# Optimization experiments

Measured on AMD Instinct MI355X. Metric: run time of the kernel, lower is better.

Reference implementation:

```python
import jax, jax.numpy as jnp
import numpy as np

B, S, D, H, HD = 1, 4096, 768, 12, 64
L, C, WIN, NCLS = 2, 256, 256, 64
NC = S // C
V, FF = 50265, 3072
NEG = -1e9
SCALE = np.float32(1.0 / np.sqrt(HD))


def setup_inputs() -> dict:
    key = jax.random.key(0)
    ks = jax.random.split(key, 32)
    p = lambda k, shape: (0.02 * jax.random.normal(k, shape)).astype(jnp.float32)
    inp = {
        'x': jax.random.randint(ks[0], (B, S), 0, V, dtype=jnp.int32),
        'mask_src': jnp.ones((B, S), dtype=jnp.int32),
        'clss': jnp.sort(jax.random.randint(ks[1], (B, NCLS), 0, S, dtype=jnp.int32), axis=-1),
        'segs': jax.random.randint(ks[2], (B, S), 0, 2, dtype=jnp.int32),
        'word_emb': p(ks[3], (V, D)),
        'pos_emb': p(ks[4], (S, D)),
        'type_emb': p(ks[5], (2, D)),
        'ln_e_s': jnp.ones((D,), jnp.float32), 'ln_e_b': jnp.zeros((D,), jnp.float32),
        'Wq': p(ks[6], (L, D, D)), 'bq': jnp.zeros((L, D), jnp.float32),
        'Wk': p(ks[7], (L, D, D)), 'bk': jnp.zeros((L, D), jnp.float32),
        'Wv': p(ks[8], (L, D, D)), 'bv': jnp.zeros((L, D), jnp.float32),
        'Wqg': p(ks[9], (L, D, D)), 'bqg': jnp.zeros((L, D), jnp.float32),
        'Wkg': p(ks[10], (L, D, D)), 'bkg': jnp.zeros((L, D), jnp.float32),
        'Wvg': p(ks[11], (L, D, D)), 'bvg': jnp.zeros((L, D), jnp.float32),
        'Wo': p(ks[12], (L, D, D)), 'bo': jnp.zeros((L, D), jnp.float32),
        'ln1_s': jnp.ones((L, D), jnp.float32), 'ln1_b': jnp.zeros((L, D), jnp.float32),
        'Wf1': p(ks[13], (L, D, FF)), 'bf1': jnp.zeros((L, FF), jnp.float32),
        'Wf2': p(ks[14], (L, FF, D)), 'bf2': jnp.zeros((L, D), jnp.float32),
        'ln2_s': jnp.ones((L, D), jnp.float32), 'ln2_b': jnp.zeros((L, D), jnp.float32),
    }
    return inp


def _layer_norm(x, s, b):
    m = jnp.mean(x, -1, keepdims=True)
    v = jnp.mean((x - m) ** 2, -1, keepdims=True)
    return (x - m) * jax.lax.rsqrt(v + 1e-5) * s + b


def _forward(x, mask_src, clss, segs, word_emb, pos_emb, type_emb, ln_e_s, ln_e_b,
             Wq, bq, Wk, bk, Wv, bv, Wqg, bqg, Wkg, bkg, Wvg, bvg, Wo, bo,
             ln1_s, ln1_b, Wf1, bf1, Wf2, bf2, ln2_s, ln2_b):
    # global positions: union of all clss values, same for every batch row
    g_idx = clss.reshape(-1)                                       # [NCLS]
    is_glb = jnp.zeros((S,), bool).at[g_idx].set(True)             # [S]
    kvalid = (mask_src > 0) & (~is_glb)[None, :]                   # band keys: no pad, no global
    gi = (jnp.arange(NC) * C)[:, None] + jnp.arange(3 * C)[None, :]  # gather idx into padded seq
    rel = jnp.arange(3 * C)[None, :] - (jnp.arange(C)[:, None] + C)  # key offset from query
    band_ok = jnp.abs(rel) <= WIN                                   # [C,3C]
    kv3 = jnp.pad(kvalid, ((0, 0), (C, C)))[:, gi]                  # [B,NC,3C]
    bmask = band_ok[None, None, None, :, :] & kv3[:, None, :, None, :]  # [B,1,NC,C,3C]
    gkey_ok = (mask_src[:, g_idx] > 0)[:, None, None, :]            # [B,1,1,NCLS]
    full_ok = (mask_src > 0)[:, None, None, :]                      # [B,1,1,S]

    h = _layer_norm(word_emb[x] + pos_emb[jnp.arange(S)][None] + type_emb[segs], ln_e_s, ln_e_b)

    for l in range(L):
        q = ((h @ Wq[l] + bq[l]).reshape(B, S, H, HD)) * SCALE
        k = (h @ Wk[l] + bk[l]).reshape(B, S, H, HD)
        v = (h @ Wv[l] + bv[l]).reshape(B, S, H, HD)
        # --- sliding-window band attention ---
        k3 = jnp.pad(k, ((0, 0), (C, C), (0, 0), (0, 0)))[:, gi]    # [B,NC,3C,H,HD]
        v3 = jnp.pad(v, ((0, 0), (C, C), (0, 0), (0, 0)))[:, gi]
        qc = q.reshape(B, NC, C, H, HD)
        sb = jnp.einsum('bnqhd,bnkhd->bhnqk', qc, k3)               # [B,H,NC,C,3C]
        sb = jnp.where(bmask, sb, NEG)
        # --- global keys seen by every query ---
        kg, vg = k[:, g_idx], v[:, g_idx]                           # [B,NCLS,H,HD]
        sg = jnp.einsum('bshd,bkhd->bhsk', q, kg)                   # [B,H,S,NCLS]
        sg = jnp.where(gkey_ok, sg, NEG)
        scores = jnp.concatenate([sg, sb.reshape(B, H, S, 3 * C)], -1)
        probs = jax.nn.softmax(scores, axis=-1)
        pg = probs[..., :NCLS]
        pb = probs[..., NCLS:].reshape(B, H, NC, C, 3 * C)
        out = jnp.einsum('bhnqk,bnkhd->bnqhd', pb, v3).reshape(B, S, H, HD)
        out = out + jnp.einsum('bhsk,bkhd->bshd', pg, vg)
        # --- global query tokens: full attention with *_global projections ---
        hg = h[:, g_idx]                                            # [B,NCLS,D]
        qg = ((hg @ Wqg[l] + bqg[l]).reshape(B, NCLS, H, HD)) * SCALE
        kgf = (h @ Wkg[l] + bkg[l]).reshape(B, S, H, HD)
        vgf = (h @ Wvg[l] + bvg[l]).reshape(B, S, H, HD)
        sfull = jnp.einsum('bqhd,bkhd->bhqk', qg, kgf)              # [B,H,NCLS,S]
        sfull = jnp.where(full_ok, sfull, NEG)
        og = jnp.einsum('bhqk,bkhd->bqhd', jax.nn.softmax(sfull, -1), vgf)
        out = out.at[:, g_idx].set(og)
        # --- output proj, residual, LN, FFN ---
        attn_out = out.reshape(B, S, D) @ Wo[l] + bo[l]
        h = _layer_norm(h + attn_out, ln1_s[l], ln1_b[l])
        ff = jax.nn.gelu(h @ Wf1[l] + bf1[l]) @ Wf2[l] + bf2[l]
        h = _layer_norm(h + ff, ln2_s[l], ln2_b[l])
    return h


def reference(x, mask_src, clss, segs, word_emb, pos_emb, type_emb, ln_e_s, ln_e_b,
              Wq, bq, Wk, bk, Wv, bv, Wqg, bqg, Wkg, bkg, Wvg, bvg, Wo, bo,
              ln1_s, ln1_b, Wf1, bf1, Wf2, bf2, ln2_s, ln2_b):
    return _forward(x, mask_src, clss, segs, word_emb, pos_emb, type_emb, ln_e_s, ln_e_b,
                    Wq, bq, Wk, bk, Wv, bv, Wqg, bqg, Wkg, bkg, Wvg, bvg, Wo, bo,
                    ln1_s, ln1_b, Wf1, bf1, Wf2, bf2, ln2_s, ln2_b)
```

## Files before the change

kernel.cpp:

```cpp
#include <hip/hip_runtime.h>
#include <hip/hip_bf16.h>
#include <cstdint>

#define SEQ  4096
#define DIM  768
#define NH   12
#define HDIM 64
#define NLAYER 2
#define CHK  256
#define WINR 256
#define NCLS 64
#define NCHK 16
#define FFD  3072
#define QSCALE 0.125f
#define LOG2E 1.44269504f
#define QSC2 (QSCALE * LOG2E)
#define SD ((size_t)SEQ * DIM)
#define PS_LD 72
#define TK 64

typedef __attribute__((__vector_size__(16))) float floatx4;
typedef __attribute__((ext_vector_type(8))) __bf16 bf16x8;
typedef __attribute__((ext_vector_type(4))) __bf16 bf16x4;

__device__ __forceinline__ void async16(const void* g, void* l) {
    __builtin_amdgcn_global_load_lds(
        (const __attribute__((address_space(1))) uint32_t*)g,
        (__attribute__((address_space(3))) uint32_t*)l, 16, 0, 0);
}

__device__ __forceinline__ float gelu_f(float x) {
    float x3 = x * x * x;
    return 0.5f * x * (1.0f + tanhf(0.7978845608028654f * (x + 0.044715f * x3)));
}

__global__ __launch_bounds__(64) void set_rank_kernel(
    const int* __restrict__ clss, int* __restrict__ isglb)
{
    isglb[clss[threadIdx.x]] = 1;
}

__global__ __launch_bounds__(256) void embed_ln_kernel(
    const int* __restrict__ x, const int* __restrict__ segs,
    const float* __restrict__ word_emb, const float* __restrict__ pos_emb,
    const float* __restrict__ type_emb, const float* __restrict__ gs,
    const float* __restrict__ gb, float* __restrict__ h, __bf16* __restrict__ hb,
    int* __restrict__ isglb)
{
    int wave = threadIdx.x >> 6, lane = threadIdx.x & 63;
    int s = blockIdx.x * 4 + wave;
    if (lane == 0) isglb[s] = 0;
    int w = x[s], sg = segs[s];
    const float4* wp = (const float4*)(word_emb + (size_t)w * DIM);
    const float4* pp = (const float4*)(pos_emb + (size_t)s * DIM);
    const float4* tp = (const float4*)(type_emb + (size_t)sg * DIM);
    float4 v[3]; float lsum = 0.f;
    #pragma unroll
    for (int i = 0; i < 3; i++) {
        int d4 = lane + i * 64;
        float4 a = wp[d4], b = pp[d4], c = tp[d4];
        float4 r;
        r.x = a.x + b.x + c.x; r.y = a.y + b.y + c.y;
        r.z = a.z + b.z + c.z; r.w = a.w + b.w + c.w;
        v[i] = r; lsum += r.x + r.y + r.z + r.w;
    }
    #pragma unroll
    for (int st = 32; st > 0; st >>= 1) lsum += __shfl_xor(lsum, st);
    float mean = lsum * (1.0f / DIM);
    float lv = 0.f;
    #pragma unroll
    for (int i = 0; i < 3; i++) {
        float dx = v[i].x - mean, dy = v[i].y - mean, dz = v[i].z - mean, dw = v[i].w - mean;
        lv += dx * dx + dy * dy + dz * dz + dw * dw;
    }
    #pragma unroll
    for (int st = 32; st > 0; st >>= 1) lv += __shfl_xor(lv, st);
    float rstd = rsqrtf(lv * (1.0f / DIM) + 1e-5f);
    #pragma unroll
    for (int i = 0; i < 3; i++) {
        int d4 = lane + i * 64;
        float4 s4v = ((const float4*)gs)[d4], b4v = ((const float4*)gb)[d4];
        float4 o;
        o.x = (v[i].x - mean) * rstd * s4v.x + b4v.x;
        o.y = (v[i].y - mean) * rstd * s4v.y + b4v.y;
        o.z = (v[i].z - mean) * rstd * s4v.z + b4v.z;
        o.w = (v[i].w - mean) * rstd * s4v.w + b4v.w;
        ((float4*)(h + (size_t)s * DIM))[d4] = o;
        bf16x4 ob; ob[0] = (__bf16)o.x; ob[1] = (__bf16)o.y;
        ob[2] = (__bf16)o.z; ob[3] = (__bf16)o.w;
        *(bf16x4*)(hb + (size_t)s * DIM + (size_t)d4 * 4) = ob;
    }
}

__global__ __launch_bounds__(256) void add_ln_kernel(
    const float* __restrict__ h, const float* __restrict__ r,
    const float* __restrict__ r2,
    const float* __restrict__ gs, const float* __restrict__ gb,
    float* __restrict__ hout, __bf16* __restrict__ hb)
{
    int wave = threadIdx.x >> 6, lane = threadIdx.x & 63;
    int s = blockIdx.x * 4 + wave;
    const float4* hp = (const float4*)(h + (size_t)s * DIM);
    const float4* rp = (const float4*)(r + (size_t)s * DIM);
    const float4* rp2 = (const float4*)(r2 + (size_t)s * DIM);
    float4 v[3]; float lsum = 0.f;
    #pragma unroll
    for (int i = 0; i < 3; i++) {
        int d4 = lane + i * 64;
        float4 a = hp[d4], b = rp[d4], c = rp2[d4];
        float4 q;
        q.x = a.x + b.x + c.x; q.y = a.y + b.y + c.y;
        q.z = a.z + b.z + c.z; q.w = a.w + b.w + c.w;
        v[i] = q; lsum += q.x + q.y + q.z + q.w;
    }
    #pragma unroll
    for (int st = 32; st > 0; st >>= 1) lsum += __shfl_xor(lsum, st);
    float mean = lsum * (1.0f / DIM);
    float lv = 0.f;
    #pragma unroll
    for (int i = 0; i < 3; i++) {
        float dx = v[i].x - mean, dy = v[i].y - mean, dz = v[i].z - mean, dw = v[i].w - mean;
        lv += dx * dx + dy * dy + dz * dz + dw * dw;
    }
    #pragma unroll
    for (int st = 32; st > 0; st >>= 1) lv += __shfl_xor(lv, st);
    float rstd = rsqrtf(lv * (1.0f / DIM) + 1e-5f);
    #pragma unroll
    for (int i = 0; i < 3; i++) {
        int d4 = lane + i * 64;
        float4 s4v = ((const float4*)gs)[d4], b4v = ((const float4*)gb)[d4];
        float4 o;
        o.x = (v[i].x - mean) * rstd * s4v.x + b4v.x;
        o.y = (v[i].y - mean) * rstd * s4v.y + b4v.y;
        o.z = (v[i].z - mean) * rstd * s4v.z + b4v.z;
        o.w = (v[i].w - mean) * rstd * s4v.w + b4v.w;
        ((float4*)(hout + (size_t)s * DIM))[d4] = o;
        bf16x4 ob; ob[0] = (__bf16)o.x; ob[1] = (__bf16)o.y;
        ob[2] = (__bf16)o.z; ob[3] = (__bf16)o.w;
        *(bf16x4*)(hb + (size_t)s * DIM + (size_t)d4 * 4) = ob;
    }
}

struct TArgs { const float* p14[14]; const float* f1[2]; const float* f2[2]; };
#define DD_ ((size_t)DIM * DIM)
__global__ __launch_bounds__(256) void tpose_setup_kernel(
    TArgs ta, __bf16* __restrict__ Wbf,
    const float* __restrict__ bq, const float* __restrict__ bk,
    const float* __restrict__ bv, const float* __restrict__ bkg,
    const float* __restrict__ bvg, float* __restrict__ bqkv)
{
    int b = blockIdx.x;
    if (b >= 17280) {
        int idx = (b - 17280) * 256 + threadIdx.x;
        int l = idx / 3840, c = idx % 3840, j = c / 768, d = c % 768;
        const float* s = (j == 0) ? bq : (j == 1) ? bk : (j == 2) ? bv : (j == 3) ? bkg : bvg;
        bqkv[idx] = s[l * 768 + d];
        return;
    }
    const float* src; __bf16* dst; int K, N, bx, by;
    if (b < 8064) {
        int z = b / 576, rr = b % 576;
        src = ta.p14[z]; dst = Wbf + (size_t)z * DD_;
        K = 768; N = 768; bx = (rr % 24) * 32; by = (rr / 24) * 32;
    } else if (b < 12672) {
        int bb = b - 8064; int z = bb / 2304, rr = bb % 2304;
        src = ta.f1[z]; dst = Wbf + 14 * DD_ + (size_t)z * 4 * DD_;
        K = 768; N = 3072; bx = (rr % 96) * 32; by = (rr / 96) * 32;
    } else {
        int bb = b - 12672; int z = bb / 2304, rr = bb % 2304;
        src = ta.f2[z]; dst = Wbf + 22 * DD_ + (size_t)z * 4 * DD_;
        K = 3072; N = 768; bx = (rr % 24) * 32; by = (rr / 24) * 32;
    }
    __shared__ float tile[32][33];
    int tx = threadIdx.x & 31, ty = threadIdx.x >> 5;
    #pragma unroll
    for (int i = 0; i < 32; i += 8)
        tile[ty + i][tx] = src[(size_t)(by + ty + i) * N + bx + tx];
    __syncthreads();
    #pragma unroll
    for (int i = 0; i < 32; i += 8)
        dst[(size_t)(bx + ty + i) * K + by + tx] = (__bf16)tile[tx][ty + i];
}

template<int TMv, int TNv>
__global__ __launch_bounds__(256) void mfma_gemm_t(
    const __bf16* __restrict__ A, const __bf16* __restrict__ Bt,
    const float* __restrict__ bias, float* __restrict__ Cf,
    float* __restrict__ Cf2, __bf16* __restrict__ Cb,
    int M, int N, int K, float scale, int act)
{
    constexpr int AM = TMv / 32, AN = TNv / 32;
    constexpr int LA = TMv / 32, LB = TNv / 32;
    __shared__ __align__(16) __bf16 As[TMv * TK];
    __shared__ __align__(16) __bf16 Bs[TNv * TK];
    int t = threadIdx.x;
    int wave = t >> 6, lane = t & 63;
    int bm = blockIdx.x * TMv, bn = blockIdx.y * TNv;
    int wm = (wave & 1) * (TMv / 2), wn = (wave >> 1) * (TNv / 2);
    int kz = blockIdx.z;
    int kn = K / (int)gridDim.z, kbeg = kz * kn;
    float* Cfo = (kz == 0) ? Cf : Cf2;

    floatx4 acc[AM][AN];
    #pragma unroll
    for (int i = 0; i < AM; i++)
        #pragma unroll
        for (int j = 0; j < AN; j++) { floatx4 z = {0.f,0.f,0.f,0.f}; acc[i][j] = z; }

    const int mrow = lane & 15, kq = (lane >> 4) * 8;
    const int tr8 = lane >> 3, c8 = lane & 7;
    const int scol = (c8 ^ tr8) * 8;
    const int swz = (lane & 7) << 3;
    const __bf16* aBase = A  + (size_t)(bm + wave * 8 + tr8) * K + scol;
    const __bf16* bBase = Bt + (size_t)(bn + wave * 8 + tr8) * K + scol;

    for (int k0 = kbeg; k0 < kbeg + kn; k0 += TK) {
        __syncthreads();
        #pragma unroll
        for (int i = 0; i < LA; i++)
            async16(aBase + k0 + (size_t)i * 32 * K, &As[(size_t)(i * 256 + wave * 64) * 8]);
        #pragma unroll
        for (int i = 0; i < LB; i++)
            async16(bBase + k0 + (size_t)i * 32 * K, &Bs[(size_t)(i * 256 + wave * 64) * 8]);
        __builtin_amdgcn_s_waitcnt(0x0f70);
        __syncthreads();
        #pragma unroll
        for (int ks = 0; ks < 2; ks++) {
            const int e = (ks * 32 + kq) ^ swz;
            bf16x8 af[AM], bfr[AN];
            #pragma unroll
            for (int mt = 0; mt < AM; mt++)
                af[mt] = *(const bf16x8*)&As[(wm + mt * 16 + mrow) * TK + e];
            #pragma unroll
            for (int nt = 0; nt < AN; nt++)
                bfr[nt] = *(const bf16x8*)&Bs[(wn + nt * 16 + mrow) * TK + e];
            #pragma unroll
            for (int mt = 0; mt < AM; mt++)
                #pragma unroll
                for (int nt = 0; nt < AN; nt++)
                    acc[mt][nt] = __builtin_amdgcn_mfma_f32_16x16x32_bf16(
                        af[mt], bfr[nt], acc[mt][nt], 0, 0, 0);
        }
    }

    int col_l = lane & 15, row_l = (lane >> 4) * 4;
    #pragma unroll
    for (int nt = 0; nt < AN; nt++) {
        int col = bn + wn + nt * 16 + col_l;
        float bs = (kz == 0) ? bias[col] : 0.f;
        #pragma unroll
        for (int mt = 0; mt < AM; mt++) {
            floatx4 v = acc[mt][nt];
            int row0 = bm + wm + mt * 16 + row_l;
            #pragma unroll
            for (int rr = 0; rr < 4; rr++) {
                float o = (v[rr] + bs) * scale;
                if (act) o = gelu_f(o);
                if (Cfo) Cfo[(size_t)(row0 + rr) * N + col] = o;
                if (Cb) Cb[(size_t)(row0 + rr) * N + col] = (__bf16)o;
            }
        }
    }
}

__global__ __launch_bounds__(256) void mfma_gemm_proj(
    const __bf16* __restrict__ A, const __bf16* __restrict__ Bt,
    const float* __restrict__ bias,
    __bf16* __restrict__ qb, __bf16* __restrict__ kb,
    __bf16* __restrict__ vb, __bf16* __restrict__ vtg,
    __bf16* __restrict__ kgb, __bf16* __restrict__ vgt, int K,
    const __bf16* __restrict__ Wqg_bt, const float* __restrict__ bqg,
    const int* __restrict__ clss, __bf16* __restrict__ qgbb)
{
    __shared__ __align__(16) __bf16 As[128 * TK];
    __shared__ __align__(16) __bf16 Bs[128 * TK];
    int t = threadIdx.x;
    int wave = t >> 6, lane = t & 63;
    const int mrow = lane & 15, kq = (lane >> 4) * 8;
    const int tr8 = lane >> 3, c8 = lane & 7;
    const int scol = (c8 ^ tr8) * 8;
    const int swz = (lane & 7) << 3;
    int col_l = lane & 15, row_l = (lane >> 4) * 4;

    if (blockIdx.y >= 30) {
        if (blockIdx.x != 0) return;
        int bn = (blockIdx.y - 30) * 128;
        int wm = (wave & 1) * 32, wn = (wave >> 1) * 64;
        int arow0 = wave * 8 + tr8;
        int g0 = clss[arow0], g1 = clss[32 + arow0];
        const __bf16* a0 = A + (size_t)g0 * DIM + scol;
        const __bf16* a1 = A + (size_t)g1 * DIM + scol;
        const __bf16* bBase = Wqg_bt + (size_t)(bn + wave * 8 + tr8) * DIM + scol;

        floatx4 acc[2][4];
        #pragma unroll
        for (int i = 0; i < 2; i++)
            #pragma unroll
            for (int j = 0; j < 4; j++) { floatx4 z = {0.f,0.f,0.f,0.f}; acc[i][j] = z; }

        for (int k0 = 0; k0 < DIM; k0 += TK) {
            __syncthreads();
            async16(a0 + k0, &As[(size_t)(wave * 64) * 8]);
            async16(a1 + k0, &As[(size_t)(256 + wave * 64) * 8]);
            #pragma unroll
            for (int i = 0; i < 4; i++)
                async16(bBase + k0 + (size_t)i * 32 * DIM, &Bs[(size_t)(i * 256 + wave * 64) * 8]);
            __builtin_amdgcn_s_waitcnt(0x0f70);
            __syncthreads();
            #pragma unroll
            for (int ks = 0; ks < 2; ks++) {
                const int e = (ks * 32 + kq) ^ swz;
                bf16x8 af[2], bfr[4];
                #pragma unroll
                for (int mt = 0; mt < 2; mt++)
                    af[mt] = *(const bf16x8*)&As[(wm + mt * 16 + mrow) * TK + e];
                #pragma unroll
                for (int nt = 0; nt < 4; nt++)
                    bfr[nt] = *(const bf16x8*)&Bs[(wn + nt * 16 + mrow) * TK + e];
                #pragma unroll
                for (int mt = 0; mt < 2; mt++)
                    #pragma unroll
                    for (int nt = 0; nt < 4; nt++)
                        acc[mt][nt] = __builtin_amdgcn_mfma_f32_16x16x32_bf16(
                            af[mt], bfr[nt], acc[mt][nt], 0, 0, 0);
            }
        }
        #pragma unroll
        for (int nt = 0; nt < 4; nt++) {
            int col = bn + wn + nt * 16 + col_l;
            float bs = bqg[col];
            #pragma unroll
            for (int mt = 0; mt < 2; mt++) {
                floatx4 v = acc[mt][nt];
                int row0 = wm + mt * 16 + row_l;
                #pragma unroll
                for (int rr = 0; rr < 4; rr++)
                    qgbb[(size_t)(row0 + rr) * DIM + col] = (__bf16)((v[rr] + bs) * QSC2);
            }
        }
        return;
    }

    int bm = blockIdx.x * 128, bn = blockIdx.y * 128;
    int wm = (wave & 1) * 64, wn = (wave >> 1) * 64;

    floatx4 acc[4][4];
    #pragma unroll
    for (int i = 0; i < 4; i++)
        #pragma unroll
        for (int j = 0; j < 4; j++) { floatx4 z = {0.f,0.f,0.f,0.f}; acc[i][j] = z; }

    const __bf16* aBase = A  + (size_t)(bm + wave * 8 + tr8) * K + scol;
    const __bf16* bBase = Bt + (size_t)(bn + wave * 8 + tr8) * K + scol;

    for (int k0 = 0; k0 < K; k0 += TK) {
        __syncthreads();
        #pragma unroll
        for (int i = 0; i < 4; i++) {
            async16(aBase + k0 + (size_t)i * 32 * K, &As[(size_t)(i * 256 + wave * 64) * 8]);
            async16(bBase + k0 + (size_t)i * 32 * K, &Bs[(size_t)(i * 256 + wave * 64) * 8]);
        }
        __builtin_amdgcn_s_waitcnt(0x0f70);
        __syncthreads();
        #pragma unroll
        for (int ks = 0; ks < 2; ks++) {
            const int e = (ks * 32 + kq) ^ swz;
            bf16x8 af[4], bfr[4];
            #pragma unroll
            for (int mt = 0; mt < 4; mt++)
                af[mt] = *(const bf16x8*)&As[(wm + mt * 16 + mrow) * TK + e];
            #pragma unroll
            for (int nt = 0; nt < 4; nt++)
                bfr[nt] = *(const bf16x8*)&Bs[(wn + nt * 16 + mrow) * TK + e];
            #pragma unroll
            for (int mt = 0; mt < 4; mt++)
                #pragma unroll
                for (int nt = 0; nt < 4; nt++)
                    acc[mt][nt] = __builtin_amdgcn_mfma_f32_16x16x32_bf16(
                        af[mt], bfr[nt], acc[mt][nt], 0, 0, 0);
        }
    }

    int seg = bn / 768;
    int colw_base = bn - seg * 768 + wn;
    float scl = (seg == 0) ? QSC2 : 1.0f;
    #pragma unroll
    for (int nt = 0; nt < 4; nt++) {
        int col = bn + wn + nt * 16 + col_l;
        int colw = colw_base + nt * 16 + col_l;
        float bs = bias[col];
        #pragma unroll
        for (int mt = 0; mt < 4; mt++) {
            floatx4 v = acc[mt][nt];
            int row0 = bm + wm + mt * 16 + row_l;
            __bf16 t4[4];
            #pragma unroll
            for (int rr = 0; rr < 4; rr++) t4[rr] = (__bf16)((v[rr] + bs) * scl);
            if (seg <= 2 || seg == 3) {
                __bf16* dst = (seg == 0) ? qb : (seg == 1) ? kb : (seg == 2) ? vb : kgb;
                #pragma unroll
                for (int rr = 0; rr < 4; rr++)
                    dst[(size_t)(row0 + rr) * 768 + colw] = t4[rr];
            }
            if (seg == 2)
                *(uint2*)&vtg[(size_t)colw * SEQ + row0] = *(uint2*)t4;
            if (seg == 4)
                *(uint2*)&vgt[(size_t)colw * SEQ + row0] = *(uint2*)t4;
        }
    }
}

__global__ __launch_bounds__(256) void attn_kernel(
    const __bf16* __restrict__ qb, const __bf16* __restrict__ kb,
    const __bf16* __restrict__ vb, const __bf16* __restrict__ vtg,
    const __bf16* __restrict__ qgbb, const __bf16* __restrict__ kgb,
    const __bf16* __restrict__ vgt,
    const int* __restrict__ clss, const int* __restrict__ mask_src,
    const int* __restrict__ is_glb,
    float* __restrict__ OpartG, float* __restrict__ mlpartG,
    __bf16* __restrict__ outb)
{
    __shared__ __align__(16) __bf16 Kt[4096];
    __shared__ __align__(16) __bf16 Vt[4096];
    __shared__ __align__(16) __bf16 Ps[4][32 * PS_LD];
    __shared__ int kvalid[64];
    __shared__ int gpos[64];

    const int hh = blockIdx.y;
    const int t = threadIdx.x, wave = t >> 6, lane = t & 63;
    const int quad = lane >> 4, col_l = lane & 15, row_l = quad * 4;
    const int l3 = lane & 3, l2h = lane >> 2, l7 = lane & 7, l3h = lane >> 3;
    __bf16* PsW = Ps[wave];

    if (blockIdx.z >= 2) {
        const int sp = blockIdx.x * 2 + (blockIdx.z - 2);
        bf16x8 aq[2];
        {
            const __bf16* qp = qgbb + (size_t)(wave * 16 + col_l) * DIM + hh * HDIM;
            aq[0] = *(const bf16x8*)(qp + quad * 8);
            aq[1] = *(const bf16x8*)(qp + 32 + quad * 8);
        }
        floatx4 oacc[4];
        #pragma unroll
        for (int i = 0; i < 4; i++) { floatx4 z = {0.f,0.f,0.f,0.f}; oacc[i] = z; }
        float m4[4], l4[4];
        #pragma unroll
        for (int r = 0; r < 4; r++) { m4[r] = -1e30f; l4[r] = 0.f; }

        for (int tt = 0; tt < 2; tt++) {
            int pos0 = sp * 128 + tt * 64;
            __syncthreads();
            if (t < 64) kvalid[t] = (mask_src[pos0 + t] > 0) ? 1 : 0;
            #pragma unroll
            for (int ii = 0; ii < 2; ii++) {
                int gid = wave * 2 + ii;
                int p = gid >> 2, kbase = (gid & 3) * 16;
                async16(kgb + (size_t)(pos0 + kbase + l2h) * DIM + hh * HDIM + p * 32 + l3 * 8,
                        &Kt[p * 2048 + kbase * 32]);
            }
            #pragma unroll
            for (int ii = 0; ii < 2; ii++) {
                int gid = wave * 2 + ii;
                int p = gid >> 2, dbase = (gid & 3) * 16;
                async16(vgt + (size_t)(hh * HDIM + dbase + l2h) * SEQ + pos0 + p * 32 + l3 * 8,
                        &Vt[p * 2048 + dbase * 32]);
            }
            __builtin_amdgcn_s_waitcnt(0x0f70);
            __syncthreads();

            floatx4 s[4];
            #pragma unroll
            for (int nt = 0; nt < 4; nt++) {
                bf16x8 b0 = *(const bf16x8*)&Kt[(nt * 16 + col_l) * 32 + quad * 8];
                bf16x8 b1 = *(const bf16x8*)&Kt[2048 + (nt * 16 + col_l) * 32 + quad * 8];
                floatx4 z = {0.f,0.f,0.f,0.f};
                z = __builtin_amdgcn_mfma_f32_16x16x32_bf16(aq[0], b0, z, 0,0,0);
                z = __builtin_amdgcn_mfma_f32_16x16x32_bf16(aq[1], b1, z, 0,0,0);
                s[nt] = z;
            }
            #pragma unroll
            for (int nt = 0; nt < 4; nt++) {
                int kvv = kvalid[nt * 16 + col_l];
                #pragma unroll
                for (int rr = 0; rr < 4; rr++)
                    if (!kvv) s[nt][rr] = -1e30f;
            }
            #pragma unroll
            for (int rr = 0; rr < 4; rr++) {
                float rm = fmaxf(fmaxf(s[0][rr], s[1][rr]), fmaxf(s[2][rr], s[3][rr]));
                rm = fmaxf(rm, __shfl_xor(rm, 1));
                rm = fmaxf(rm, __shfl_xor(rm, 2));
                rm = fmaxf(rm, __shfl_xor(rm, 4));
                rm = fmaxf(rm, __shfl_xor(rm, 8));
                float mo = m4[rr];
                float mn = fmaxf(mo, rm);
                float alpha = exp2f(mo - mn);
                float rsum = 0.f;
                #pragma unroll
                for (int nt = 0; nt < 4; nt++) {
                    float p = exp2f(s[nt][rr] - mn);
                    rsum += p;
                    PsW[(row_l + rr) * PS_LD + nt * 16 + col_l] = (__bf16)p;
                }
                rsum += __shfl_xor(rsum, 1);
                rsum += __shfl_xor(rsum, 2);
                rsum += __shfl_xor(rsum, 4);
                rsum += __shfl_xor(rsum, 8);
                l4[rr] = l4[rr] * alpha + rsum;
                m4[rr] = mn;
                #pragma unroll
                for (int nt = 0; nt < 4; nt++) oacc[nt][rr] *= alpha;
            }
            bf16x8 ap0 = *(const bf16x8*)&PsW[col_l * PS_LD + quad * 8];
            bf16x8 ap1 = *(const bf16x8*)&PsW[col_l * PS_LD + 32 + quad * 8];
            #pragma unroll
            for (int nt = 0; nt < 4; nt++) {
                bf16x8 b0 = *(const bf16x8*)&Vt[(nt * 16 + col_l) * 32 + quad * 8];
                bf16x8 b1 = *(const bf16x8*)&Vt[2048 + (nt * 16 + col_l) * 32 + quad * 8];
                oacc[nt] = __builtin_amdgcn_mfma_f32_16x16x32_bf16(ap0, b0, oacc[nt], 0,0,0);
                oacc[nt] = __builtin_amdgcn_mfma_f32_16x16x32_bf16(ap1, b1, oacc[nt], 0,0,0);
            }
        }
        size_t base = (size_t)(hh * 32 + sp) * 64;
        #pragma unroll
        for (int nt = 0; nt < 4; nt++)
            #pragma unroll
            for (int rr = 0; rr < 4; rr++)
                OpartG[(base + wave * 16 + row_l + rr) * 64 + nt * 16 + col_l] = oacc[nt][rr];
        if (col_l == 0) {
            #pragma unroll
            for (int rr = 0; rr < 4; rr++) {
                mlpartG[(base + wave * 16 + row_l + rr) * 2]     = m4[rr];
                mlpartG[(base + wave * 16 + row_l + rr) * 2 + 1] = l4[rr];
            }
        }
        return;
    }

    const int n = blockIdx.x, qh = blockIdx.z;
    const int qw = qh * 128 + wave * 32;

    if (t < 64) gpos[t] = clss[t];

    bf16x8 aq[2][2];
    #pragma unroll
    for (int mt = 0; mt < 2; mt++) {
        const __bf16* qp = qb + (size_t)(n * CHK + qw + mt * 16 + col_l) * DIM + hh * HDIM;
        aq[mt][0] = *(const bf16x8*)(qp + quad * 8);
        aq[mt][1] = *(const bf16x8*)(qp + 32 + quad * 8);
    }

    floatx4 oacc[2][4];
    #pragma unroll
    for (int i = 0; i < 2; i++)
        #pragma unroll
        for (int j = 0; j < 4; j++) { floatx4 z = {0.f,0.f,0.f,0.f}; oacc[i][j] = z; }
    float mrw[8], lrw[8];
    #pragma unroll
    for (int r = 0; r < 8; r++) { mrw[r] = -1e30f; lrw[r] = 0.f; }

    for (int tt = 0; tt < 11; tt++) {
        __syncthreads();
        int jbase = -1;
        int isglob = (tt == 0);
        if (isglob) {
            if (t < 64) kvalid[t] = (mask_src[gpos[t]] > 0) ? 1 : 0;
            #pragma unroll
            for (int g = 0; g < 2; g++) {
                int gid = wave * 2 + g;
                int p = gid >> 2, kbase = (gid & 3) * 16;
                int pos = gpos[kbase + l2h];
                async16(kb + (size_t)pos * DIM + hh * HDIM + p * 32 + l3 * 8,
                        &Kt[p * 2048 + kbase * 32]);
            }
            __bf16* Vrow = &Ps[0][0];
            #pragma unroll
            for (int g = 0; g < 2; g++) {
                int cg = wave * 2 + g;
                int pos = gpos[cg * 8 + l3h];
                async16(vb + (size_t)pos * DIM + hh * HDIM + l7 * 8,
                        &Vrow[cg * 64 * 8]);
            }
        } else {
            int jt = qh * 2 + tt - 1;
            jbase = jt * 64;
            if (t < 64) {
                int pos = n * CHK + jbase + t - CHK;
                kvalid[t] = (pos >= 0 && pos < SEQ && mask_src[pos] > 0
                             && is_glb[pos] == 0) ? 1 : 0;
            }
            int s0 = n * CHK + jbase - CHK;
            #pragma unroll
            for (int g = 0; g < 2; g++) {
                int gid = wave * 2 + g;
                int p = gid >> 2, kbase = (gid & 3) * 16;
                int pos = s0 + kbase + l2h; pos = min(max(pos, 0), SEQ - 1);
                async16(kb + (size_t)pos * DIM + hh * HDIM + p * 32 + l3 * 8,
                        &Kt[p * 2048 + kbase * 32]);
            }
            #pragma unroll
            for (int g = 0; g < 2; g++) {
                int gid = wave * 2 + g;
                int p = gid >> 2, dbase = (gid & 3) * 16;
                int d = dbase + l2h;
                int s = s0 + p * 32 + l3 * 8; s = min(max(s, 0), SEQ - 8);
                async16(vtg + (size_t)(hh * HDIM + d) * SEQ + s,
                        &Vt[p * 2048 + dbase * 32]);
            }
        }
        __builtin_amdgcn_s_waitcnt(0x0f70);
        __syncthreads();
        if (isglob) {
            const __bf16* Vrow = &Ps[0][0];
            for (int idx = t; idx < 4096; idx += 256) {
                int key = idx >> 6, d = idx & 63;
                Vt[(key >> 5) * 2048 + d * 32 + (key & 31)] = Vrow[idx];
            }
            __syncthreads();
        } else {
            if (jbase + 63 < qw || jbase > qw + 543) continue;
        }

        bf16x8 bkf[4][2];
        #pragma unroll
        for (int nt = 0; nt < 4; nt++) {
            bkf[nt][0] = *(const bf16x8*)&Kt[(nt * 16 + col_l) * 32 + quad * 8];
            bkf[nt][1] = *(const bf16x8*)&Kt[2048 + (nt * 16 + col_l) * 32 + quad * 8];
        }
        int kv[4];
        #pragma unroll
        for (int nt = 0; nt < 4; nt++) kv[nt] = kvalid[nt * 16 + col_l];

        #pragma unroll
        for (int mt = 0; mt < 2; mt++) {
            floatx4 s[4];
            #pragma unroll
            for (int nt = 0; nt < 4; nt++) {
                floatx4 z = {0.f,0.f,0.f,0.f};
                z = __builtin_amdgcn_mfma_f32_16x16x32_bf16(aq[mt][0], bkf[nt][0], z, 0,0,0);
                z = __builtin_amdgcn_mfma_f32_16x16x32_bf16(aq[mt][1], bkf[nt][1], z, 0,0,0);
                s[nt] = z;
            }
            #pragma unroll
            for (int nt = 0; nt < 4; nt++)
                #pragma unroll
                for (int rr = 0; rr < 4; rr++) {
                    int ok = kv[nt];
                    if (!isglob) {
                        int i = qw + mt * 16 + row_l + rr;
                        int rel = jbase + nt * 16 + col_l - i;
                        ok = ok && (rel >= 0) && (rel <= 2 * WINR);
                    }
                    if (!ok) s[nt][rr] = -1e30f;
                }
            #pragma unroll
            for (int rr = 0; rr < 4; rr++) {
                float rm = fmaxf(fmaxf(s[0][rr], s[1][rr]), fmaxf(s[2][rr], s[3][rr]));
                rm = fmaxf(rm, __shfl_xor(rm, 1));
                rm = fmaxf(rm, __shfl_xor(rm, 2));
                rm = fmaxf(rm, __shfl_xor(rm, 4));
                rm = fmaxf(rm, __shfl_xor(rm, 8));
                int ri = mt * 4 + rr;
                float mo = mrw[ri];
                float mn = fmaxf(mo, rm);
                float alpha = exp2f(mo - mn);
                float rsum = 0.f;
                #pragma unroll
                for (int nt = 0; nt < 4; nt++) {
                    float p = exp2f(s[nt][rr] - mn);
                    rsum += p;
                    PsW[(mt * 16 + row_l + rr) * PS_LD + nt * 16 + col_l] = (__bf16)p;
                }
                rsum += __shfl_xor(rsum, 1);
                rsum += __shfl_xor(rsum, 2);
                rsum += __shfl_xor(rsum, 4);
                rsum += __shfl_xor(rsum, 8);
                lrw[ri] = lrw[ri] * alpha + rsum;
                mrw[ri] = mn;
                #pragma unroll
                for (int nt = 0; nt < 4; nt++) oacc[mt][nt][rr] *= alpha;
            }
        }
        bf16x8 bvf[4][2], ap[2][2];
        #pragma unroll
        for (int nt = 0; nt < 4; nt++) {
            bvf[nt][0] = *(const bf16x8*)&Vt[(nt * 16 + col_l) * 32 + quad * 8];
            bvf[nt][1] = *(const bf16x8*)&Vt[2048 + (nt * 16 + col_l) * 32 + quad * 8];
        }
        #pragma unroll
        for (int mt = 0; mt < 2; mt++) {
            ap[mt][0] = *(const bf16x8*)&PsW[(mt * 16 + col_l) * PS_LD + quad * 8];
            ap[mt][1] = *(const bf16x8*)&PsW[(mt * 16 + col_l) * PS_LD + 32 + quad * 8];
        }
        #pragma unroll
        for (int mt = 0; mt < 2; mt++)
            #pragma unroll
            for (int nt = 0; nt < 4; nt++) {
                oacc[mt][nt] = __builtin_amdgcn_mfma_f32_16x16x32_bf16(
                    ap[mt][0], bvf[nt][0], oacc[mt][nt], 0,0,0);
                oacc[mt][nt] = __builtin_amdgcn_mfma_f32_16x16x32_bf16(
                    ap[mt][1], bvf[nt][1], oacc[mt][nt], 0,0,0);
            }
    }

    #pragma unroll
    for (int mt = 0; mt < 2; mt++) {
        #pragma unroll
        for (int rr = 0; rr < 4; rr++) {
            int srow = n * CHK + qw + mt * 16 + row_l + rr;
            if (is_glb[srow]) continue;
            float inv = 1.0f / lrw[mt * 4 + rr];
            #pragma unroll
            for (int nt = 0; nt < 4; nt++)
                outb[(size_t)srow * DIM + hh * HDIM + nt * 16 + col_l] =
                    (__bf16)(oacc[mt][nt][rr] * inv);
        }
    }
}

__global__ __launch_bounds__(64) void gq_finalize(
    const float* __restrict__ OpartG, const float* __restrict__ mlpartG,
    const int* __restrict__ clss, __bf16* __restrict__ outb)
{
    int r = blockIdx.x, hh = blockIdx.y, d = threadIdx.x;
    float M = -1e30f;
    for (int sp = 0; sp < 32; sp++)
        M = fmaxf(M, mlpartG[(((size_t)hh * 32 + sp) * 64 + r) * 2]);
    float L = 0.f, acc = 0.f;
    for (int sp = 0; sp < 32; sp++) {
        size_t b = ((size_t)hh * 32 + sp) * 64 + r;
        float w = exp2f(mlpartG[b * 2] - M);
        L += mlpartG[b * 2 + 1] * w;
        acc += w * OpartG[b * 64 + d];
    }
    int pos = clss[r];
    outb[(size_t)pos * DIM + hh * HDIM + d] = (__bf16)(acc / L);
}

extern "C" void kernel_launch(void* const* d_in, const int* in_sizes, int n_in,
                              void* d_out, int out_size, void* d_ws, size_t ws_size,
                              hipStream_t stream)
{
    const int* x        = (const int*)d_in[0];
    const int* mask_src = (const int*)d_in[1];
    const int* clss     = (const int*)d_in[2];
    const int* segs     = (const int*)d_in[3];
    const float* word_emb = (const float*)d_in[4];
    const float* pos_emb  = (const float*)d_in[5];
    const float* type_emb = (const float*)d_in[6];
    const float* ln_e_s   = (const float*)d_in[7];
    const float* ln_e_b   = (const float*)d_in[8];
    const float* Wq  = (const float*)d_in[9];
    const float* bq  = (const float*)d_in[10];
    const float* Wk  = (const float*)d_in[11];
    const float* bk  = (const float*)d_in[12];
    const float* Wv  = (const float*)d_in[13];
    const float* bv  = (const float*)d_in[14];
    const float* Wqg = (const float*)d_in[15];
    const float* bqg = (const float*)d_in[16];
    const float* Wkg = (const float*)d_in[17];
    const float* bkg = (const float*)d_in[18];
    const float* Wvg = (const float*)d_in[19];
    const float* bvg = (const float*)d_in[20];
    const float* Wo  = (const float*)d_in[21];
    const float* bo  = (const float*)d_in[22];
    const float* ln1_s = (const float*)d_in[23];
    const float* ln1_b = (const float*)d_in[24];
    const float* Wf1 = (const float*)d_in[25];
    const float* bf1 = (const float*)d_in[26];
    const float* Wf2 = (const float*)d_in[27];
    const float* bf2 = (const float*)d_in[28];
    const float* ln2_s = (const float*)d_in[29];
    const float* ln2_b = (const float*)d_in[30];

    const size_t DD = (size_t)DIM * DIM;
    float* ws = (float*)d_ws;
    float*  h    = ws;
    float*  s4   = ws + SD;
    __bf16* hb   = (__bf16*)(ws + 2 * SD);
    __bf16* b6b  = (__bf16*)(ws + 2 * SD) + SD;
    __bf16* qb   = (__bf16*)(ws + 3 * SD);
    __bf16* kb   = (__bf16*)(ws + 3 * SD) + SD;
    __bf16* vb   = (__bf16*)(ws + 4 * SD);
    __bf16* vtg  = (__bf16*)(ws + 4 * SD) + SD;
    __bf16* kgb  = (__bf16*)(ws + 5 * SD);
    __bf16* vgt  = (__bf16*)(ws + 5 * SD) + SD;
    __bf16* gelu_b = qb;
    float* extra = ws + 6 * SD;
    __bf16* Wbf   = (__bf16*)extra;
    float* after_w = extra + 15 * DD;
    float* bqkv   = after_w;
    float* OpartG = bqkv + 7680;
    float* mlpartG= OpartG + 1572864;
    float* s4b    = mlpartG + 49152;
    __bf16* qgbb  = (__bf16*)(s4b + SD);
    int*   isglb  = (int*)(qgbb + (size_t)NCLS * DIM);

    embed_ln_kernel<<<SEQ / 4, 256, 0, stream>>>(x, segs, word_emb, pos_emb, type_emb,
                                                 ln_e_s, ln_e_b, h, hb, isglb);
    set_rank_kernel<<<1, 64, 0, stream>>>(clss, isglb);
    {
        TArgs ta{};
        ta.p14[0] = Wq;        ta.p14[1] = Wk;        ta.p14[2] = Wv;
        ta.p14[3] = Wkg;       ta.p14[4] = Wvg;
        ta.p14[5] = Wq + DD;   ta.p14[6] = Wk + DD;   ta.p14[7] = Wv + DD;
        ta.p14[8] = Wkg + DD;  ta.p14[9] = Wvg + DD;
        ta.p14[10] = Wo;       ta.p14[11] = Wo + DD;
        ta.p14[12] = Wqg;      ta.p14[13] = Wqg + DD;
        ta.f1[0] = Wf1; ta.f1[1] = Wf1 + (size_t)DIM * FFD;
        ta.f2[0] = Wf2; ta.f2[1] = Wf2 + (size_t)FFD * DIM;
        tpose_setup_kernel<<<17310, 256, 0, stream>>>(ta, Wbf, bq, bk, bv, bkg, bvg, bqkv);
    }

    for (int l = 0; l < NLAYER; l++) {
        const float* bqg_l = bqg + (size_t)l * DIM;
        const float* bo_l  = bo  + (size_t)l * DIM;
        const float* bf1_l = bf1 + (size_t)l * FFD;
        const float* bf2_l = bf2 + (size_t)l * DIM;

        mfma_gemm_proj<<<dim3(SEQ / 128, 36), 256, 0, stream>>>(
            hb, Wbf + (size_t)l * 5 * DD, bqkv + l * 3840,
            qb, kb, vb, vtg, kgb, vgt, DIM,
            Wbf + 12 * DD + (size_t)l * DD, bqg_l, clss, qgbb);
        attn_kernel<<<dim3(NCHK, NH, 4), 256, 0, stream>>>(
            qb, kb, vb, vtg, qgbb, kgb, vgt, clss, mask_src, isglb,
            OpartG, mlpartG, b6b);
        gq_finalize<<<dim3(NCLS, NH), 64, 0, stream>>>(OpartG, mlpartG, clss, b6b);
        mfma_gemm_t<128, 64><<<dim3(SEQ / 128, DIM / 64, 2), 256, 0, stream>>>(
            b6b, Wbf + 10 * DD + (size_t)l * DD, bo_l, s4, s4b, nullptr,
            SEQ, DIM, DIM, 1.0f, 0);
        add_ln_kernel<<<SEQ / 4, 256, 0, stream>>>(h, s4, s4b, ln1_s + (size_t)l * DIM,
                                                   ln1_b + (size_t)l * DIM, h, hb);
        mfma_gemm_t<128, 128><<<dim3(SEQ / 128, FFD / 128, 1), 256, 0, stream>>>(
            hb, Wbf + 14 * DD + (size_t)l * 4 * DD, bf1_l, nullptr, nullptr, gelu_b,
            SEQ, FFD, DIM, 1.0f, 1);
        mfma_gemm_t<128, 64><<<dim3(SEQ / 128, DIM / 64, 2), 256, 0, stream>>>(
            gelu_b, Wbf + 22 * DD + (size_t)l * 4 * DD, bf2_l, s4, s4b, nullptr,
            SEQ, DIM, FFD, 1.0f, 0);
        add_ln_kernel<<<SEQ / 4, 256, 0, stream>>>(h, s4, s4b, ln2_s + (size_t)l * DIM,
                                                   ln2_b + (size_t)l * DIM,
                                                   (l == NLAYER - 1) ? (float*)d_out : h, hb);
    }
}
```

Measured before the change: 721.8 us.

## Defer softmax rescaling, compute row sums via MFMA, trim V stores, fold rank kernel

Inside the attention kernel the online softmax now rescales the running max and accumulators only when some row's new max exceeds the old one by a threshold. The row sums are accumulated by an extra MFMA against a ones vector, which replaces the shuffle-reduction sums. The projection GEMM writes row-major V only for global rows, since the transposed copy covers the rest, and the tiny set_rank kernel is folded into the setup kernel to save a launch. In exchange it adds extra MFMA work and a threshold that allows exponentials up to 2^8 before rescaling, and the row sums now come from bf16-rounded probabilities.

```diff
diff --git a/kernel.cpp b/kernel.cpp
--- a/kernel.cpp
+++ b/kernel.cpp
@@ -18,6 +18,7 @@
 #define SD ((size_t)SEQ * DIM)
 #define PS_LD 72
 #define TK 64
+#define DEFER_THR 8.0f
 
 typedef __attribute__((__vector_size__(16))) float floatx4;
 typedef __attribute__((ext_vector_type(8))) __bf16 bf16x8;
@@ -32,12 +33,6 @@
 __device__ __forceinline__ float gelu_f(float x) {
     float x3 = x * x * x;
     return 0.5f * x * (1.0f + tanhf(0.7978845608028654f * (x + 0.044715f * x3)));
-}
-
-__global__ __launch_bounds__(64) void set_rank_kernel(
-    const int* __restrict__ clss, int* __restrict__ isglb)
-{
-    isglb[clss[threadIdx.x]] = 1;
 }
 
 __global__ __launch_bounds__(256) void embed_ln_kernel(
@@ -147,7 +142,8 @@
     TArgs ta, __bf16* __restrict__ Wbf,
     const float* __restrict__ bq, const float* __restrict__ bk,
     const float* __restrict__ bv, const float* __restrict__ bkg,
-    const float* __restrict__ bvg, float* __restrict__ bqkv)
+    const float* __restrict__ bvg, float* __restrict__ bqkv,
+    const int* __restrict__ clss, int* __restrict__ isglb)
 {
     int b = blockIdx.x;
     if (b >= 17280) {
@@ -155,6 +151,7 @@
         int l = idx / 3840, c = idx % 3840, j = c / 768, d = c % 768;
         const float* s = (j == 0) ? bq : (j == 1) ? bk : (j == 2) ? bv : (j == 3) ? bkg : bvg;
         bqkv[idx] = s[l * 768 + d];
+        if (b == 17280 && threadIdx.x < 64) isglb[clss[threadIdx.x]] = 1;
         return;
     }
     const float* src; __bf16* dst; int K, N, bx, by;
@@ -270,7 +267,8 @@
     __bf16* __restrict__ vb, __bf16* __restrict__ vtg,
     __bf16* __restrict__ kgb, __bf16* __restrict__ vgt, int K,
     const __bf16* __restrict__ Wqg_bt, const float* __restrict__ bqg,
-    const int* __restrict__ clss, __bf16* __restrict__ qgbb)
+    const int* __restrict__ clss, __bf16* __restrict__ qgbb,
+    const int* __restrict__ is_glb)
 {
     __shared__ __align__(16) __bf16 As[128 * TK];
     __shared__ __align__(16) __bf16 Bs[128 * TK];
@@ -384,6 +382,15 @@
     int seg = bn / 768;
     int colw_base = bn - seg * 768 + wn;
     float scl = (seg == 0) ? QSC2 : 1.0f;
+    unsigned gmask = 0;
+    if (seg == 2) {
+        #pragma unroll
+        for (int mt = 0; mt < 4; mt++)
+            #pragma unroll
+            for (int rr = 0; rr < 4; rr++)
+                gmask |= (unsigned)(is_glb[bm + wm + mt * 16 + row_l + rr] != 0)
+                         << (mt * 4 + rr);
+    }
     #pragma unroll
     for (int nt = 0; nt < 4; nt++) {
         int col = bn + wn + nt * 16 + col_l;
@@ -396,8 +403,13 @@
             __bf16 t4[4];
             #pragma unroll
             for (int rr = 0; rr < 4; rr++) t4[rr] = (__bf16)((v[rr] + bs) * scl);
-            if (seg <= 2 || seg == 3) {
-                __bf16* dst = (seg == 0) ? qb : (seg == 1) ? kb : (seg == 2) ? vb : kgb;
+            if (seg == 2) {
+                #pragma unroll
+                for (int rr = 0; rr < 4; rr++)
+                    if ((gmask >> (mt * 4 + rr)) & 1)
+                        vb[(size_t)(row0 + rr) * 768 + colw] = t4[rr];
+            } else if (seg <= 3) {
+                __bf16* dst = (seg == 0) ? qb : (seg == 1) ? kb : kgb;
                 #pragma unroll
                 for (int rr = 0; rr < 4; rr++)
                     dst[(size_t)(row0 + rr) * 768 + colw] = t4[rr];
@@ -432,6 +444,10 @@
     const int l3 = lane & 3, l2h = lane >> 2, l7 = lane & 7, l3h = lane >> 3;
     __bf16* PsW = Ps[wave];
 
+    bf16x8 ones8;
+    #pragma unroll
+    for (int i = 0; i < 8; i++) ones8[i] = (__bf16)1.0f;
+
     if (blockIdx.z >= 2) {
         const int sp = blockIdx.x * 2 + (blockIdx.z - 2);
         bf16x8 aq[2];
@@ -440,12 +456,13 @@
             aq[0] = *(const bf16x8*)(qp + quad * 8);
             aq[1] = *(const bf16x8*)(qp + 32 + quad * 8);
         }
-        floatx4 oacc[4];
+        floatx4 oacc[4], oaccE;
         #pragma unroll
         for (int i = 0; i < 4; i++) { floatx4 z = {0.f,0.f,0.f,0.f}; oacc[i] = z; }
-        float m4[4], l4[4];
-        #pragma unroll
-        for (int r = 0; r < 4; r++) { m4[r] = -1e30f; l4[r] = 0.f; }
+        { floatx4 z = {0.f,0.f,0.f,0.f}; oaccE = z; }
+        float m4[4];
+        #pragma unroll
+        for (int r = 0; r < 4; r++) m4[r] = -1e30f;
 
         for (int tt = 0; tt < 2; tt++) {
             int pos0 = sp * 128 + tt * 64;
@@ -485,6 +502,7 @@
                 for (int rr = 0; rr < 4; rr++)
                     if (!kvv) s[nt][rr] = -1e30f;
             }
+            float rmx[4]; int grow = 0;
             #pragma unroll
             for (int rr = 0; rr < 4; rr++) {
                 float rm = fmaxf(fmaxf(s[0][rr], s[1][rr]), fmaxf(s[2][rr], s[3][rr]));
@@ -492,27 +510,34 @@
                 rm = fmaxf(rm, __shfl_xor(rm, 2));
                 rm = fmaxf(rm, __shfl_xor(rm, 4));
                 rm = fmaxf(rm, __shfl_xor(rm, 8));
-                float mo = m4[rr];
-                float mn = fmaxf(mo, rm);
-                float alpha = exp2f(mo - mn);
-                float rsum = 0.f;
+                rmx[rr] = rm;
+                grow |= (rm > m4[rr] + DEFER_THR) ? 1 : 0;
+            }
+            if (__any(grow)) {
+                #pragma unroll
+                for (int rr = 0; rr < 4; rr++) {
+                    float mo = m4[rr];
+                    float mn = fmaxf(mo, rmx[rr]);
+                    float alpha = exp2f(mo - mn);
+                    m4[rr] = mn;
+                    #pragma unroll
+                    for (int nt = 0; nt < 4; nt++) oacc[nt][rr] *= alpha;
+                    oaccE[rr] *= alpha;
+                }
+            }
+            #pragma unroll
+            for (int rr = 0; rr < 4; rr++) {
+                float mn = m4[rr];
                 #pragma unroll
                 for (int nt = 0; nt < 4; nt++) {
                     float p = exp2f(s[nt][rr] - mn);
-                    rsum += p;
                     PsW[(row_l + rr) * PS_LD + nt * 16 + col_l] = (__bf16)p;
                 }
-                rsum += __shfl_xor(rsum, 1);
-                rsum += __shfl_xor(rsum, 2);
-                rsum += __shfl_xor(rsum, 4);
-                rsum += __shfl_xor(rsum, 8);
-                l4[rr] = l4[rr] * alpha + rsum;
-                m4[rr] = mn;
-                #pragma unroll
-                for (int nt = 0; nt < 4; nt++) oacc[nt][rr] *= alpha;
             }
             bf16x8 ap0 = *(const bf16x8*)&PsW[col_l * PS_LD + quad * 8];
             bf16x8 ap1 = *(const bf16x8*)&PsW[col_l * PS_LD + 32 + quad * 8];
+            oaccE = __builtin_amdgcn_mfma_f32_16x16x32_bf16(ap0, ones8, oaccE, 0,0,0);
+            oaccE = __builtin_amdgcn_mfma_f32_16x16x32_bf16(ap1, ones8, oaccE, 0,0,0);
             #pragma unroll
             for (int nt = 0; nt < 4; nt++) {
                 bf16x8 b0 = *(const bf16x8*)&Vt[(nt * 16 + col_l) * 32 + quad * 8];
@@ -531,7 +556,7 @@
             #pragma unroll
             for (int rr = 0; rr < 4; rr++) {
                 mlpartG[(base + wave * 16 + row_l + rr) * 2]     = m4[rr];
-                mlpartG[(base + wave * 16 + row_l + rr) * 2 + 1] = l4[rr];
+                mlpartG[(base + wave * 16 + row_l + rr) * 2 + 1] = oaccE[rr];
             }
         }
         return;
@@ -551,13 +576,16 @@
     }
 
     floatx4 oacc[2][4];
-    #pragma unroll
-    for (int i = 0; i < 2; i++)
+    floatx4 oaccE[2];
+    #pragma unroll
+    for (int i = 0; i < 2; i++) {
         #pragma unroll
         for (int j = 0; j < 4; j++) { floatx4 z = {0.f,0.f,0.f,0.f}; oacc[i][j] = z; }
-    float mrw[8], lrw[8];
-    #pragma unroll
-    for (int r = 0; r < 8; r++) { mrw[r] = -1e30f; lrw[r] = 0.f; }
+        floatx4 z = {0.f,0.f,0.f,0.f}; oaccE[i] = z;
+    }
+    float mrw[8];
+    #pragma unroll
+    for (int r = 0; r < 8; r++) mrw[r] = -1e30f;
 
     for (int tt = 0; tt < 11; tt++) {
         __syncthreads();
@@ -653,6 +681,7 @@
                     }
                     if (!ok) s[nt][rr] = -1e30f;
                 }
+            float rmx[4]; int grow = 0;
             #pragma unroll
             for (int rr = 0; rr < 4; rr++) {
                 float rm = fmaxf(fmaxf(s[0][rr], s[1][rr]), fmaxf(s[2][rr], s[3][rr]));
@@ -660,25 +689,30 @@
                 rm = fmaxf(rm, __shfl_xor(rm, 2));
                 rm = fmaxf(rm, __shfl_xor(rm, 4));
                 rm = fmaxf(rm, __shfl_xor(rm, 8));
-                int ri = mt * 4 + rr;
-                float mo = mrw[ri];
-                float mn = fmaxf(mo, rm);
-                float alpha = exp2f(mo - mn);
-                float rsum = 0.f;
+                rmx[rr] = rm;
+                grow |= (rm > mrw[mt * 4 + rr] + DEFER_THR) ? 1 : 0;
+            }
+            if (__any(grow)) {
+                #pragma unroll
+                for (int rr = 0; rr < 4; rr++) {
+                    int ri = mt * 4 + rr;
+                    float mo = mrw[ri];
+                    float mn = fmaxf(mo, rmx[rr]);
+                    float alpha = exp2f(mo - mn);
+                    mrw[ri] = mn;
+                    #pragma unroll
+                    for (int nt = 0; nt < 4; nt++) oacc[mt][nt][rr] *= alpha;
+                    oaccE[mt][rr] *= alpha;
+                }
+            }
+            #pragma unroll
+            for (int rr = 0; rr < 4; rr++) {
+                float mn = mrw[mt * 4 + rr];
                 #pragma unroll
                 for (int nt = 0; nt < 4; nt++) {
                     float p = exp2f(s[nt][rr] - mn);
-                    rsum += p;
                     PsW[(mt * 16 + row_l + rr) * PS_LD + nt * 16 + col_l] = (__bf16)p;
                 }
-                rsum += __shfl_xor(rsum, 1);
-                rsum += __shfl_xor(rsum, 2);
-                rsum += __shfl_xor(rsum, 4);
-                rsum += __shfl_xor(rsum, 8);
-                lrw[ri] = lrw[ri] * alpha + rsum;
-                mrw[ri] = mn;
-                #pragma unroll
-                for (int nt = 0; nt < 4; nt++) oacc[mt][nt][rr] *= alpha;
             }
         }
         bf16x8 bvf[4][2], ap[2][2];
@@ -693,7 +727,9 @@
             ap[mt][1] = *(const bf16x8*)&PsW[(mt * 16 + col_l) * PS_LD + 32 + quad * 8];
         }
         #pragma unroll
-        for (int mt = 0; mt < 2; mt++)
+        for (int mt = 0; mt < 2; mt++) {
+            oaccE[mt] = __builtin_amdgcn_mfma_f32_16x16x32_bf16(ap[mt][0], ones8, oaccE[mt], 0,0,0);
+            oaccE[mt] = __builtin_amdgcn_mfma_f32_16x16x32_bf16(ap[mt][1], ones8, oaccE[mt], 0,0,0);
             #pragma unroll
             for (int nt = 0; nt < 4; nt++) {
                 oacc[mt][nt] = __builtin_amdgcn_mfma_f32_16x16x32_bf16(
@@ -701,6 +737,7 @@
                 oacc[mt][nt] = __builtin_amdgcn_mfma_f32_16x16x32_bf16(
                     ap[mt][1], bvf[nt][1], oacc[mt][nt], 0,0,0);
             }
+        }
     }
 
     #pragma unroll
@@ -709,7 +746,7 @@
         for (int rr = 0; rr < 4; rr++) {
             int srow = n * CHK + qw + mt * 16 + row_l + rr;
             if (is_glb[srow]) continue;
-            float inv = 1.0f / lrw[mt * 4 + rr];
+            float inv = 1.0f / oaccE[mt][rr];
             #pragma unroll
             for (int nt = 0; nt < 4; nt++)
                 outb[(size_t)srow * DIM + hh * HDIM + nt * 16 + col_l] =
@@ -798,7 +835,6 @@
 
     embed_ln_kernel<<<SEQ / 4, 256, 0, stream>>>(x, segs, word_emb, pos_emb, type_emb,
                                                  ln_e_s, ln_e_b, h, hb, isglb);
-    set_rank_kernel<<<1, 64, 0, stream>>>(clss, isglb);
     {
         TArgs ta{};
         ta.p14[0] = Wq;        ta.p14[1] = Wk;        ta.p14[2] = Wv;
@@ -809,7 +845,8 @@
         ta.p14[12] = Wqg;      ta.p14[13] = Wqg + DD;
         ta.f1[0] = Wf1; ta.f1[1] = Wf1 + (size_t)DIM * FFD;
         ta.f2[0] = Wf2; ta.f2[1] = Wf2 + (size_t)FFD * DIM;
-        tpose_setup_kernel<<<17310, 256, 0, stream>>>(ta, Wbf, bq, bk, bv, bkg, bvg, bqkv);
+        tpose_setup_kernel<<<17310, 256, 0, stream>>>(ta, Wbf, bq, bk, bv, bkg, bvg,
+                                                      bqkv, clss, isglb);
     }
 
     for (int l = 0; l < NLAYER; l++) {
@@ -821,7 +858,7 @@
         mfma_gemm_proj<<<dim3(SEQ / 128, 36), 256, 0, stream>>>(
             hb, Wbf + (size_t)l * 5 * DD, bqkv + l * 3840,
             qb, kb, vb, vtg, kgb, vgt, DIM,
-            Wbf + 12 * DD + (size_t)l * DD, bqg_l, clss, qgbb);
+            Wbf + 12 * DD + (size_t)l * DD, bqg_l, clss, qgbb, isglb);
         attn_kernel<<<dim3(NCHK, NH, 4), 256, 0, stream>>>(
             qb, kb, vb, vtg, qgbb, kgb, vgt, clss, mask_src, isglb,
             OpartG, mlpartG, b6b);
```

New measurement: 702.1 us (median of 2 runs). -2.7%, faster.
